# Optimization experiments

Hardware: AMD Instinct MI355X
Metric: run time of the kernel (lower is better)

## Reference

```python
import jax, jax.numpy as jnp
import numpy as np

EPSILON = 1.0
SIGMA = 1.0
SPRING_K = 0.5
BATCH, NPART, DIM = 128, 512, 3


def setup_inputs() -> dict:
    key = jax.random.key(0)
    x = jax.random.normal(key, (BATCH, NPART, DIM), dtype=jnp.float32)
    return {"x": x}


def _remove_diag(d):
    # d: (B, N, N) -> (B, N, N-1), dropping the diagonal via the flatten trick
    B, N, _ = d.shape
    return d.reshape(B, N * N)[:, 1:].reshape(B, N - 1, N + 1)[:, :, :-1].reshape(B, N, N - 1)


def reference(x):
    # x: (B, N, D)
    B, N, D = x.shape
    pair_vec = x[:, :, None, :] - x[:, None, :, :]          # (B, N, N, D)
    distances = jnp.linalg.norm(pair_vec, axis=-1)           # (B, N, N)
    distances = _remove_diag(distances)                      # (B, N, N-1)
    distances_inverse = 1.0 / distances
    pow_6 = (SIGMA * distances_inverse) ** 6
    pair_potential = EPSILON * 4.0 * (pow_6 ** 2 - pow_6)
    pair_potential = pair_potential * distances_inverse * distances
    total_potential = jnp.sum(pair_potential, axis=(-1, -2)) / 2.0  # (B,)
    # harmonic restraint about center of mass (periodic=False branch)
    com = jnp.mean(x, axis=-2, keepdims=True)
    rel = x - com
    total_potential = total_potential + 0.5 * SPRING_K * jnp.sum(rel ** 2, axis=(-1, -2))
    # forward = log_prob = -potential
    return -total_potential
```

## Files before the change

### kernel.cpp

```cpp
#include <hip/hip_runtime.h>

#define NPART 512
#define BATCH 128
#define SPLITS 8
#define KR 32
#define NTH 256

__device__ __forceinline__ void pair_term(const float4 a, const float4 b,
                                          float& acc12, float& acc6) {
    float dx = a.x - b.x, dy = a.y - b.y, dz = a.z - b.z;
    float r2 = fmaf(dx, dx, fmaf(dy, dy, dz * dz));
    float i2 = __builtin_amdgcn_rcpf(r2);
    float i6 = i2 * i2 * i2;
    acc12 = fmaf(i6, i6, acc12);
    acc6 += i6;
}

__global__ __launch_bounds__(NTH, 4) void lj_partial(
    const float* __restrict__ x, float* __restrict__ partial) {
    const int bid = blockIdx.x;
    const int b = bid >> 3;
    const int s = bid & 7;
    const int tid = threadIdx.x;

    __shared__ float4 sp[NPART + 256];
    __shared__ float wred[4];
    __shared__ float wspr[4][4];

    const float* xb = x + (size_t)b * (NPART * 3);
    float* spf = reinterpret_cast<float*>(sp);
    #pragma unroll
    for (int t = 0; t < 6; ++t) {
        const int idx = tid + t * NTH;
        const float v = xb[idx];
        const int p = idx / 3;
        const int c = idx - p * 3;
        spf[p * 4 + c] = v;
        if (p < 256) spf[(p + NPART) * 4 + c] = v;
    }
    __syncthreads();

    const int r0 = 2 * tid;
    const float4 pi0 = sp[r0];
    const float4 pi1 = sp[r0 + 1];
    const int k0 = 1 + KR * s;
    const float4* pj = &sp[r0 + k0];

    float acc6 = 0.0f, acc12 = 0.0f;

    {
        const float4 P = pj[0];
        pair_term(pi0, P, acc12, acc6);
    }
    #pragma unroll 8
    for (int kk = 1; kk < KR; ++kk) {
        const float4 P = pj[kk];
        pair_term(pi0, P, acc12, acc6);
        pair_term(pi1, P, acc12, acc6);
    }
    {
        const float4 P = pj[KR];
        pair_term(pi1, P, acc12, acc6);
    }

    if (s == SPLITS - 1) {
        {
            const float4 P = sp[r0 + 256];
            float dx = pi0.x - P.x, dy = pi0.y - P.y, dz = pi0.z - P.z;
            float r2 = fmaf(dx, dx, fmaf(dy, dy, dz * dz));
            float i2 = __builtin_amdgcn_rcpf(r2);
            float i6 = i2 * i2 * i2;
            acc12 -= 0.5f * i6 * i6;
            acc6 -= 0.5f * i6;
        }
        {
            const float4 P = sp[r0 + 1 + 256];
            float dx = pi1.x - P.x, dy = pi1.y - P.y, dz = pi1.z - P.z;
            float r2 = fmaf(dx, dx, fmaf(dy, dy, dz * dz));
            float i2 = __builtin_amdgcn_rcpf(r2);
            float i6 = i2 * i2 * i2;
            acc12 -= 0.5f * i6 * i6;
            acc6 -= 0.5f * i6;
        }
    }

    float pot = 4.0f * (acc12 - acc6);

    #pragma unroll
    for (int off = 32; off; off >>= 1) pot += __shfl_down(pot, off, 64);

    float sx = 0.0f, sy = 0.0f, sz = 0.0f, ssq = 0.0f;
    if (s == 0) {
        sx = pi0.x + pi1.x;
        sy = pi0.y + pi1.y;
        sz = pi0.z + pi1.z;
        ssq = pi0.x * pi0.x + pi0.y * pi0.y + pi0.z * pi0.z
            + pi1.x * pi1.x + pi1.y * pi1.y + pi1.z * pi1.z;
        #pragma unroll
        for (int off = 32; off; off >>= 1) {
            sx  += __shfl_down(sx,  off, 64);
            sy  += __shfl_down(sy,  off, 64);
            sz  += __shfl_down(sz,  off, 64);
            ssq += __shfl_down(ssq, off, 64);
        }
    }

    const int wave = tid >> 6;
    const int lane = tid & 63;
    if (lane == 0) {
        wred[wave] = pot;
        wspr[wave][0] = sx; wspr[wave][1] = sy;
        wspr[wave][2] = sz; wspr[wave][3] = ssq;
    }
    __syncthreads();

    if (tid == 0) {
        float P = 0.0f, SX = 0.0f, SY = 0.0f, SZ = 0.0f, SS = 0.0f;
        #pragma unroll
        for (int w = 0; w < 4; ++w) {
            P += wred[w];
            SX += wspr[w][0]; SY += wspr[w][1];
            SZ += wspr[w][2]; SS += wspr[w][3];
        }
        float res = P;
        if (s == 0) {
            res += 0.25f * (SS - (SX * SX + SY * SY + SZ * SZ) * (1.0f / NPART));
        }
        partial[bid] = res;
    }
}

__global__ void lj_combine(const float* __restrict__ partial,
                           float* __restrict__ out) {
    const int t = blockIdx.x * blockDim.x + threadIdx.x;
    if (t < BATCH) {
        float sum = 0.0f;
        #pragma unroll
        for (int i = 0; i < SPLITS; ++i) sum += partial[SPLITS * t + i];
        out[t] = -sum;
    }
}

extern "C" void kernel_launch(void* const* d_in, const int* in_sizes, int n_in,
                              void* d_out, int out_size, void* d_ws, size_t ws_size,
                              hipStream_t stream) {
    const float* x = (const float*)d_in[0];
    float* out = (float*)d_out;
    float* pw = (float*)d_ws;

    lj_partial<<<BATCH * SPLITS, NTH, 0, stream>>>(x, pw);
    lj_combine<<<1, 128, 0, stream>>>(pw, out);
}
```

Before: 14.52 us.

## Split particles into even/odd LDS halves and fuse combine via atomicAdd

```diff
diff --git a/kernel.cpp b/kernel.cpp
--- a/kernel.cpp
+++ b/kernel.cpp
@@ -3,8 +3,8 @@
 #define NPART 512
 #define BATCH 128
 #define SPLITS 8
-#define KR 32
 #define NTH 256
+
 
 __device__ __forceinline__ void pair_term(const float4 a, const float4 b,
                                           float& acc12, float& acc6) {
@@ -16,14 +16,14 @@
     acc6 += i6;
 }
 
-__global__ __launch_bounds__(NTH, 4) void lj_partial(
-    const float* __restrict__ x, float* __restrict__ partial) {
+__global__ __launch_bounds__(NTH, 4) void lj_main(
+    const float* __restrict__ x, float* __restrict__ out) {
     const int bid = blockIdx.x;
     const int b = bid >> 3;
     const int s = bid & 7;
     const int tid = threadIdx.x;
 
-    __shared__ float4 sp[NPART + 256];
+    __shared__ float4 sp[768];
     __shared__ float wred[4];
     __shared__ float wspr[4][4];
 
@@ -35,37 +35,39 @@
         const float v = xb[idx];
         const int p = idx / 3;
         const int c = idx - p * 3;
-        spf[p * 4 + c] = v;
-        if (p < 256) spf[(p + NPART) * 4 + c] = v;
+        const int sl = (p >> 1) + ((p & 1) ? 384 : 0);
+        spf[sl * 4 + c] = v;
+        if (p < 256) spf[(sl + 256) * 4 + c] = v;
     }
     __syncthreads();
 
-    const int r0 = 2 * tid;
-    const float4 pi0 = sp[r0];
-    const float4 pi1 = sp[r0 + 1];
-    const int k0 = 1 + KR * s;
-    const float4* pj = &sp[r0 + k0];
+    const float4 pi0 = sp[tid];
+    const float4 pi1 = sp[384 + tid];
+
+    const float4* base = sp + tid + 16 * s;
 
     float acc6 = 0.0f, acc12 = 0.0f;
 
-    {
-        const float4 P = pj[0];
-        pair_term(pi0, P, acc12, acc6);
-    }
-    #pragma unroll 8
-    for (int kk = 1; kk < KR; ++kk) {
-        const float4 P = pj[kk];
-        pair_term(pi0, P, acc12, acc6);
-        pair_term(pi1, P, acc12, acc6);
+    pair_term(pi0, base[384], acc12, acc6);
+    #pragma unroll
+    for (int m = 1; m <= 15; ++m) {
+        const float4 Pe = base[m];
+        pair_term(pi0, Pe, acc12, acc6);
+        pair_term(pi1, Pe, acc12, acc6);
+        const float4 Po = base[384 + m];
+        pair_term(pi0, Po, acc12, acc6);
+        pair_term(pi1, Po, acc12, acc6);
     }
     {
-        const float4 P = pj[KR];
-        pair_term(pi1, P, acc12, acc6);
+        const float4 Pe = base[16];
+        pair_term(pi0, Pe, acc12, acc6);
+        pair_term(pi1, Pe, acc12, acc6);
     }
+    pair_term(pi1, base[400], acc12, acc6);
 
     if (s == SPLITS - 1) {
         {
-            const float4 P = sp[r0 + 256];
+            const float4 P = sp[tid + 128];
             float dx = pi0.x - P.x, dy = pi0.y - P.y, dz = pi0.z - P.z;
             float r2 = fmaf(dx, dx, fmaf(dy, dy, dz * dz));
             float i2 = __builtin_amdgcn_rcpf(r2);
@@ -74,7 +76,7 @@
             acc6 -= 0.5f * i6;
         }
         {
-            const float4 P = sp[r0 + 1 + 256];
+            const float4 P = sp[tid + 512];
             float dx = pi1.x - P.x, dy = pi1.y - P.y, dz = pi1.z - P.z;
             float r2 = fmaf(dx, dx, fmaf(dy, dy, dz * dz));
             float i2 = __builtin_amdgcn_rcpf(r2);
@@ -126,18 +128,7 @@
         if (s == 0) {
             res += 0.25f * (SS - (SX * SX + SY * SY + SZ * SZ) * (1.0f / NPART));
         }
-        partial[bid] = res;
-    }
-}
-
-__global__ void lj_combine(const float* __restrict__ partial,
-                           float* __restrict__ out) {
-    const int t = blockIdx.x * blockDim.x + threadIdx.x;
-    if (t < BATCH) {
-        float sum = 0.0f;
-        #pragma unroll
-        for (int i = 0; i < SPLITS; ++i) sum += partial[SPLITS * t + i];
-        out[t] = -sum;
+        atomicAdd(&out[b], -res);
     }
 }
 
@@ -146,8 +137,7 @@
                               hipStream_t stream) {
     const float* x = (const float*)d_in[0];
     float* out = (float*)d_out;
-    float* pw = (float*)d_ws;
 
-    lj_partial<<<BATCH * SPLITS, NTH, 0, stream>>>(x, pw);
-    lj_combine<<<1, 128, 0, stream>>>(pw, out);
+    hipMemsetAsync(out, 0, BATCH * sizeof(float), stream);
+    lj_main<<<BATCH * SPLITS, NTH, 0, stream>>>(x, out);
 }
```

Measured after the change: 18.07 us. 24.5% more time.
